# Kernel optimization log

Hardware: AMD Instinct MI355X
Metric: run time of the kernel (lower is better)

The kernel has to match this reference:

```python
import jax, jax.numpy as jnp
import numpy as np

H = 16  # number of heads (from init_kwargs)
LN_EPS = 1e-5  # torch nn.LayerNorm default


def layer_norm(x, g, b, eps=LN_EPS):
    mu = jnp.mean(x, axis=-1, keepdims=True)
    var = jnp.var(x, axis=-1, keepdims=True)
    return (x - mu) * jax.lax.rsqrt(var + eps) * g + b


def setup_inputs() -> dict:
    key = jax.random.key(0)
    ks = jax.random.split(key, 8)
    B, S, d = 2, 2048, 1024
    s = 0.02  # small init scale keeps softmax logits in a sane range
    return {
        "embed": jax.random.normal(ks[0], (B, S, d), jnp.float32),
        "Wk": jax.random.normal(ks[1], (d, d), jnp.float32) * s,
        "Wq": jax.random.normal(ks[2], (d, d), jnp.float32) * s,
        "Wv": jax.random.normal(ks[3], (d, d), jnp.float32) * s,
        "w1_w": jax.random.normal(ks[4], (4 * d, d), jnp.float32) * s,
        "w1_b": jnp.zeros((4 * d,), jnp.float32),
        "w2_w": jax.random.normal(ks[5], (d, 4 * d), jnp.float32) * s,
        "w2_b": jnp.zeros((d,), jnp.float32),
        "ln_g": jnp.ones((d,), jnp.float32),
        "ln_b": jnp.zeros((d,), jnp.float32),
        "ln2_g": jnp.ones((d,), jnp.float32),
        "ln2_b": jnp.zeros((d,), jnp.float32),
    }


def reference(embed, Wk, Wq, Wv, w1_w, w1_b, w2_w, w2_b, ln_g, ln_b, ln2_g, ln2_b):
    B, S, d = embed.shape
    dh = d // H
    # nn.Linear(d, d, bias=False): y = x @ W.T
    K = embed @ Wk.T
    Q = embed @ Wq.T
    V = embed @ Wv.T
    Qh = Q.reshape(B, S, H, dh)
    Kh = K.reshape(B, S, H, dh)
    Vh = V.reshape(B, S, H, dh)
    # per-head attention, all heads batched: [B, H, S, S]
    scores = jnp.einsum('bshd,bthd->bhst', Qh, Kh) / jnp.sqrt(jnp.float32(dh))
    attn = jax.nn.softmax(scores, axis=-1)
    out = jnp.einsum('bhst,bthd->bshd', attn, Vh).reshape(B, S, d)
    out = layer_norm(out + embed, ln_g, ln_b)          # residual + ln
    hidden = jax.nn.silu(out @ w1_w.T + w1_b)          # FFN with silu gate
    out2 = hidden @ w2_w.T + w2_b
    return layer_norm(out2 + out, ln2_g, ln2_b)        # residual + ln2
```

## Files before the change

kernel.cpp:

```cpp
#include <hip/hip_runtime.h>
#include <hip/hip_bf16.h>
#include <stdint.h>

typedef __attribute__((ext_vector_type(8))) __bf16 bf16x8;
typedef __attribute__((ext_vector_type(4))) float f32x4;
typedef __attribute__((ext_vector_type(16))) float f32x16;
typedef __attribute__((ext_vector_type(8))) uint16_t u16x8;

__device__ inline uint16_t f2bf(float x) {
  union { float f; uint32_t u; } v; v.f = x;
  uint32_t r = v.u + 0x7fffu + ((v.u >> 16) & 1u);
  return (uint16_t)(r >> 16);
}
__device__ inline float bf2f(uint16_t x) {
  union { uint32_t u; float f; } v; v.u = (uint32_t)x << 16;
  return v.f;
}

#define MFMA16(a, b, c) __builtin_amdgcn_mfma_f32_16x16x32_bf16(a, b, c, 0, 0, 0)
#define MFMA32(a, b, c) __builtin_amdgcn_mfma_f32_32x32x16_bf16(a, b, c, 0, 0, 0)
#define GLOAD16(g, l) __builtin_amdgcn_global_load_lds((const __attribute__((address_space(1))) void*)(g), (__attribute__((address_space(3))) void*)(l), 16, 0, 0)

#if __has_builtin(__builtin_amdgcn_exp2f)
#define EXP2(x) __builtin_amdgcn_exp2f(x)
#else
#define EXP2(x) exp2f(x)
#endif

__device__ inline uint32_t cvtpk_bf16(float lo, float hi) {
  uint32_t r;
  asm("v_cvt_pk_bf16_f32 %0, %1, %2" : "=v"(r) : "v"(lo), "v"(hi));
  return r;
}
__device__ inline void perm32swap(uint32_t& a, uint32_t& b) {
  asm volatile("v_permlane32_swap_b32 %0, %1" : "+v"(a), "+v"(b));
}

__global__ void cast_all(const float* __restrict__ embed, const float* __restrict__ Wq,
                         const float* __restrict__ Wk, const float* __restrict__ Wv,
                         const float* __restrict__ w1w, const float* __restrict__ w2w,
                         uint16_t* __restrict__ xbf, uint16_t* __restrict__ wqkv,
                         uint16_t* __restrict__ w1b, uint16_t* __restrict__ w2b) {
  const int i = (blockIdx.x * 256 + threadIdx.x) * 4;
  const float* src; uint16_t* dst; float sc = 1.f; int off;
  if (i < 4194304)       { src = embed; dst = xbf;            off = i; }
  else if (i < 5242880)  { src = Wq;  dst = wqkv;             off = i - 4194304; sc = 0.125f * 1.44269504f; }
  else if (i < 6291456)  { src = Wk;  dst = wqkv + 1048576;   off = i - 5242880; }
  else if (i < 7340032)  { src = Wv;  dst = wqkv + 2097152;   off = i - 6291456; }
  else if (i < 11534336) { src = w1w; dst = w1b;              off = i - 7340032; }
  else                   { src = w2w; dst = w2b;              off = i - 11534336; }
  float4 v = *(const float4*)(src + off);
  ushort4 o;
  o.x = f2bf(v.x * sc); o.y = f2bf(v.y * sc);
  o.z = f2bf(v.z * sc); o.w = f2bf(v.w * sc);
  *(ushort4*)(dst + off) = o;
}

template <int EPI>
__global__ void gemm_bt(const uint16_t* __restrict__ A, const uint16_t* __restrict__ Bm,
                        void* __restrict__ C0, void* __restrict__ C1,
                        void* __restrict__ C2, void* __restrict__ C3,
                        const float* __restrict__ bias, int N, int K, int ldk) {
  __shared__ uint16_t Albs[128 * 64];
  __shared__ uint16_t Blbs[128 * 64];
  const int tid = threadIdx.x;
  const int l = tid & 63, w = tid >> 6;
  const int wr = w >> 1, wc = w & 1;

  const int orig = blockIdx.y * gridDim.x + blockIdx.x;
  const int xcd = orig & 7;
  const int j = orig >> 3;
  const int cols_per = gridDim.y >> 1;
  const int row0 = ((xcd & 3) * 8 + (j & 7)) * 128;
  const int col0 = ((xcd >> 2) * cols_per + (j >> 3)) * 128;

  const int kz = blockIdx.z;
  const uint16_t* Ap = A + (size_t)kz * K;
  const uint16_t* Bp = Bm + (size_t)kz * K;
  void* Co = kz == 0 ? C0 : (kz == 1 ? C1 : (kz == 2 ? C2 : C3));

  const int srow8 = l >> 3;
  const int sgcol = ((l & 7) ^ srow8) * 8;
  const int lr = l & 15, l4 = l >> 4;

  f32x4 acc[4][4] = {};

  const int nk = K >> 6;
  for (int kt = 0; kt < nk; ++kt) {
    __syncthreads();
    const int k0 = kt * 64 + sgcol;
#pragma unroll
    for (int i = 0; i < 4; ++i) {
      GLOAD16(Ap + (size_t)(row0 + i * 32 + w * 8 + srow8) * ldk + k0,
              Albs + (i * 32 + w * 8) * 64);
      GLOAD16(Bp + (size_t)(col0 + i * 32 + w * 8 + srow8) * ldk + k0,
              Blbs + (i * 32 + w * 8) * 64);
    }
    __syncthreads();
#pragma unroll
    for (int kk = 0; kk < 2; ++kk) {
      bf16x8 af[4], bfr[4];
#pragma unroll
      for (int m = 0; m < 4; ++m) {
        const int r = wr * 64 + m * 16 + lr;
        af[m] = *(const bf16x8*)((const char*)Albs + r * 128 + (((kk * 4 + l4) ^ (r & 7)) << 4));
      }
#pragma unroll
      for (int n = 0; n < 4; ++n) {
        const int r = wc * 64 + n * 16 + lr;
        bfr[n] = *(const bf16x8*)((const char*)Blbs + r * 128 + (((kk * 4 + l4) ^ (r & 7)) << 4));
      }
#pragma unroll
      for (int m = 0; m < 4; ++m)
#pragma unroll
        for (int n = 0; n < 4; ++n)
          acc[m][n] = MFMA16(af[m], bfr[n], acc[m][n]);
    }
  }

  float bias_r[4];
  if (EPI == 1) {
#pragma unroll
    for (int n = 0; n < 4; ++n) bias_r[n] = bias[col0 + wc * 64 + n * 16 + lr];
  }
#pragma unroll
  for (int m = 0; m < 4; ++m)
#pragma unroll
    for (int n = 0; n < 4; ++n) {
      const int rbase = row0 + wr * 64 + m * 16 + (l4 << 2);
      const int c = col0 + wc * 64 + n * 16 + lr;
      if (EPI == 1) {
#pragma unroll
        for (int v = 0; v < 4; ++v) {
          float x = acc[m][n][v] + bias_r[n];
          float s = x / (1.f + __expf(-x));
          ((uint16_t*)Co)[(size_t)(rbase + v) * N + c] = f2bf(s);
        }
      } else if (EPI == 2) {
#pragma unroll
        for (int v = 0; v < 4; ++v)
          ((uint16_t*)Co)[(size_t)(rbase + v) * N + c] = f2bf(acc[m][n][v]);
      } else {
        if (c < 2048) {
#pragma unroll
          for (int v = 0; v < 4; ++v)
            ((uint16_t*)C0)[(size_t)(rbase + v) * 2048 + c] = f2bf(acc[m][n][v]);
        } else {
          const int d = c - 2048;
          union { uint16_t u[4]; uint64_t q; } pk;
#pragma unroll
          for (int v = 0; v < 4; ++v) pk.u[v] = f2bf(acc[m][n][v]);
          const int bb = rbase >> 11, srow = rbase & 2047;
          uint16_t* vt = (uint16_t*)C1;
          *(uint64_t*)(vt + ((size_t)((bb << 4) + (d >> 6)) * 64 + (d & 63)) * 2048 + srow) = pk.q;
        }
      }
    }
}

__global__ __launch_bounds__(256, 2) void attn_kernel(const uint16_t* __restrict__ qk,
                                                      const uint16_t* __restrict__ Vt,
                                                      uint16_t* __restrict__ Op0,
                                                      uint16_t* __restrict__ Op1,
                                                      float* __restrict__ lsum) {
  __shared__ uint16_t Klds[2][4096];
  __shared__ uint16_t Vlds[2][4096];
  const int tid = threadIdx.x;
  const int l = tid & 63, w = tid >> 6;
  const int lq = l & 31, hi = l >> 5;
  const int qt = ((blockIdx.y & 7) << 1) | (blockIdx.x >> 3);
  const int bh = ((blockIdx.x & 7) << 2) | (blockIdx.y >> 3);
  const int z = blockIdx.z;
  const size_t rowbase = (size_t)(bh >> 4) * 2048;
  const int h = bh & 15;
  const int hq = h * 64, hk = 1024 + h * 64;
  const int kvbase = z * 1024;
  uint16_t* Op = z ? Op1 : Op0;

  const int qrow = qt * 128 + w * 32 + lq;
  bf16x8 qf[4];
  {
    const uint16_t* qp = qk + (rowbase + qrow) * 2048 + hq + hi * 8;
#pragma unroll
    for (int c = 0; c < 4; ++c) qf[c] = *(const bf16x8*)(qp + c * 16);
  }

  const int srow = w * 8 + (l >> 3);
  const int gcol = 8 * ((l & 7) ^ (l >> 3));

  f32x16 ot[2];
#pragma unroll
  for (int r = 0; r < 16; ++r) { ot[0][r] = 0.f; ot[1][r] = 0.f; }
  float l_run = 0.f;

  auto STAGE = [&](int buf, int kv0) {
#pragma unroll
    for (int p = 0; p < 2; ++p) {
      const uint16_t* srcK = qk + (rowbase + kv0 + p * 32 + srow) * 2048 + hk + gcol;
      GLOAD16(srcK, (char*)&Klds[buf][0] + p * 4096 + w * 1024);
      const uint16_t* srcV = Vt + ((size_t)bh * 64 + p * 32 + srow) * 2048 + kv0 + gcol;
      GLOAD16(srcV, (char*)&Vlds[buf][0] + p * 4096 + w * 1024);
    }
  };

  STAGE(0, kvbase);
  int cur = 0;
  const int swz = (lq & 7) << 4;

  for (int t = 0; t < 16; ++t) {
    asm volatile("s_waitcnt vmcnt(0)" ::: "memory");
    __builtin_amdgcn_s_barrier();
    if (t < 15) STAGE(cur ^ 1, kvbase + (t + 1) * 64);

    f32x16 st[2];
#pragma unroll
    for (int b = 0; b < 2; ++b) {
      f32x16 acm;
#pragma unroll
      for (int r = 0; r < 16; ++r) acm[r] = 0.f;
      __builtin_amdgcn_s_setprio(1);
#pragma unroll
      for (int c = 0; c < 4; ++c) {
        const int cbk = (c * 32 + hi * 16) ^ swz;
        bf16x8 kf = *(const bf16x8*)((const char*)&Klds[cur][0] + (b * 32 + lq) * 128 + cbk);
        acm = MFMA32(kf, qf[c], acm);
      }
      __builtin_amdgcn_s_setprio(0);
      st[b] = acm;
    }

    float rsum = 0.f;
#pragma unroll
    for (int b = 0; b < 2; ++b)
#pragma unroll
      for (int r = 0; r < 16; ++r) {
        float e = EXP2(st[b][r]);
        st[b][r] = e;
        rsum += e;
      }
    l_run += rsum + __shfl_xor(rsum, 32, 64);

    uint32_t pa[4][4];
#pragma unroll
    for (int b = 0; b < 2; ++b)
#pragma unroll
      for (int c = 0; c < 2; ++c) {
        uint32_t a0 = cvtpk_bf16(st[b][8 * c + 0], st[b][8 * c + 1]);
        uint32_t a1 = cvtpk_bf16(st[b][8 * c + 2], st[b][8 * c + 3]);
        uint32_t b0 = cvtpk_bf16(st[b][8 * c + 4], st[b][8 * c + 5]);
        uint32_t b1 = cvtpk_bf16(st[b][8 * c + 6], st[b][8 * c + 7]);
        perm32swap(a0, b0);
        perm32swap(a1, b1);
        pa[b * 2 + c][0] = a0; pa[b * 2 + c][1] = a1;
        pa[b * 2 + c][2] = b0; pa[b * 2 + c][3] = b1;
      }

    __builtin_amdgcn_s_setprio(1);
#pragma unroll
    for (int ks = 0; ks < 4; ++ks) {
      bf16x8 pf = *(bf16x8*)&pa[ks][0];
#pragma unroll
      for (int db = 0; db < 2; ++db) {
        const int cbk = (ks * 32 + hi * 16) ^ swz;
        bf16x8 vf = *(const bf16x8*)((const char*)&Vlds[cur][0] + (db * 32 + lq) * 128 + cbk);
        ot[db] = MFMA32(vf, pf, ot[db]);
      }
    }
    __builtin_amdgcn_s_setprio(0);
    cur ^= 1;
  }

  uint16_t* orow = Op + (rowbase + qrow) * 1024 + h * 64;
#pragma unroll
  for (int db = 0; db < 2; ++db)
#pragma unroll
    for (int m = 0; m < 4; ++m) {
      union { uint16_t u[4]; uint64_t q; } pk;
#pragma unroll
      for (int v = 0; v < 4; ++v) pk.u[v] = f2bf(ot[db][4 * m + v]);
      *(uint64_t*)(orow + db * 32 + 8 * m + 4 * hi) = pk.q;
    }
  if (l < 32) lsum[(size_t)(z * 32 + bh) * 2048 + qrow] = l_run;
}

__global__ __launch_bounds__(256) void ln1_fused(const uint16_t* __restrict__ O0,
                                                 const uint16_t* __restrict__ O1,
                                                 const float* __restrict__ lsum,
                                                 const float* __restrict__ embed,
                                                 const float* __restrict__ g,
                                                 const float* __restrict__ b,
                                                 uint16_t* __restrict__ ybf) {
  const int row = blockIdx.x;
  const int t = threadIdx.x;
  const int l = t & 63, w = t >> 6;
  const int bb = row >> 11, q = row & 2047;
  const int bh = bb * 16 + (t >> 4);
  const float l0 = lsum[(size_t)bh * 2048 + q];
  const float l1 = lsum[(size_t)(32 + bh) * 2048 + q];
  const float linv = 1.f / (l0 + l1);
  ushort4 a = *((const ushort4*)(O0 + (size_t)row * 1024) + t);
  ushort4 c = *((const ushort4*)(O1 + (size_t)row * 1024) + t);
  float4 e = *((const float4*)(embed + (size_t)row * 1024) + t);
  float x0 = (bf2f(a.x) + bf2f(c.x)) * linv + e.x;
  float x1 = (bf2f(a.y) + bf2f(c.y)) * linv + e.y;
  float x2 = (bf2f(a.z) + bf2f(c.z)) * linv + e.z;
  float x3 = (bf2f(a.w) + bf2f(c.w)) * linv + e.w;
  float s = x0 + x1 + x2 + x3;
  float qq = x0 * x0 + x1 * x1 + x2 * x2 + x3 * x3;
#pragma unroll
  for (int off = 1; off < 64; off <<= 1) {
    s += __shfl_xor(s, off, 64);
    qq += __shfl_xor(qq, off, 64);
  }
  __shared__ float red[8];
  if (l == 0) { red[w] = s; red[w + 4] = qq; }
  __syncthreads();
  s = red[0] + red[1] + red[2] + red[3];
  qq = red[4] + red[5] + red[6] + red[7];
  const float mu = s * (1.f / 1024.f);
  const float var = qq * (1.f / 1024.f) - mu * mu;
  const float rstd = rsqrtf(var + 1e-5f);
  float4 vg = *((const float4*)g + t);
  float4 vbb = *((const float4*)b + t);
  union { uint16_t u[4]; uint64_t v; } o;
  o.u[0] = f2bf((x0 - mu) * rstd * vg.x + vbb.x);
  o.u[1] = f2bf((x1 - mu) * rstd * vg.y + vbb.y);
  o.u[2] = f2bf((x2 - mu) * rstd * vg.z + vbb.z);
  o.u[3] = f2bf((x3 - mu) * rstd * vg.w + vbb.w);
  *((uint64_t*)(ybf + (size_t)row * 1024) + t) = o.v;
}

__global__ __launch_bounds__(256) void ln_kernel(const uint16_t* __restrict__ x0b,
                                                 const uint16_t* __restrict__ xb1,
                                                 const uint16_t* __restrict__ xb2,
                                                 const uint16_t* __restrict__ xb3,
                                                 const uint16_t* __restrict__ xb4,
                                                 const float* __restrict__ abias,
                                                 const float* __restrict__ g,
                                                 const float* __restrict__ b,
                                                 float* __restrict__ y32) {
  const int row = blockIdx.x;
  const int t = threadIdx.x;
  const int l = t & 63, w = t >> 6;
  ushort4 v0 = *((const ushort4*)(x0b + (size_t)row * 1024) + t);
  float x0 = bf2f(v0.x), x1 = bf2f(v0.y), x2 = bf2f(v0.z), x3 = bf2f(v0.w);
  {
    ushort4 vb4 = *((const ushort4*)(xb1 + (size_t)row * 1024) + t);
    x0 += bf2f(vb4.x); x1 += bf2f(vb4.y); x2 += bf2f(vb4.z); x3 += bf2f(vb4.w);
  }
  {
    ushort4 vb4 = *((const ushort4*)(xb2 + (size_t)row * 1024) + t);
    x0 += bf2f(vb4.x); x1 += bf2f(vb4.y); x2 += bf2f(vb4.z); x3 += bf2f(vb4.w);
  }
  {
    ushort4 vb4 = *((const ushort4*)(xb3 + (size_t)row * 1024) + t);
    x0 += bf2f(vb4.x); x1 += bf2f(vb4.y); x2 += bf2f(vb4.z); x3 += bf2f(vb4.w);
  }
  {
    ushort4 vb4 = *((const ushort4*)(xb4 + (size_t)row * 1024) + t);
    x0 += bf2f(vb4.x); x1 += bf2f(vb4.y); x2 += bf2f(vb4.z); x3 += bf2f(vb4.w);
  }
  {
    float4 vb = *((const float4*)abias + t);
    x0 += vb.x; x1 += vb.y; x2 += vb.z; x3 += vb.w;
  }
  float s = x0 + x1 + x2 + x3;
  float q = x0 * x0 + x1 * x1 + x2 * x2 + x3 * x3;
#pragma unroll
  for (int off = 1; off < 64; off <<= 1) {
    s += __shfl_xor(s, off, 64);
    q += __shfl_xor(q, off, 64);
  }
  __shared__ float red[8];
  if (l == 0) { red[w] = s; red[w + 4] = q; }
  __syncthreads();
  s = red[0] + red[1] + red[2] + red[3];
  q = red[4] + red[5] + red[6] + red[7];
  const float mu = s * (1.f / 1024.f);
  const float var = q * (1.f / 1024.f) - mu * mu;
  const float rstd = rsqrtf(var + 1e-5f);
  float4 vg = *((const float4*)g + t);
  float4 vbb = *((const float4*)b + t);
  float y0 = (x0 - mu) * rstd * vg.x + vbb.x;
  float y1 = (x1 - mu) * rstd * vg.y + vbb.y;
  float y2 = (x2 - mu) * rstd * vg.z + vbb.z;
  float y3 = (x3 - mu) * rstd * vg.w + vbb.w;
  *((float4*)(y32 + (size_t)row * 1024) + t) = make_float4(y0, y1, y2, y3);
}

extern "C" void kernel_launch(void* const* d_in, const int* in_sizes, int n_in,
                              void* d_out, int out_size, void* d_ws, size_t ws_size,
                              hipStream_t stream) {
  const float* embed = (const float*)d_in[0];
  const float* Wk = (const float*)d_in[1];
  const float* Wq = (const float*)d_in[2];
  const float* Wv = (const float*)d_in[3];
  const float* w1w = (const float*)d_in[4];
  const float* w1bias = (const float*)d_in[5];
  const float* w2w = (const float*)d_in[6];
  const float* w2bias = (const float*)d_in[7];
  const float* lng = (const float*)d_in[8];
  const float* lnb = (const float*)d_in[9];
  const float* ln2g = (const float*)d_in[10];
  const float* ln2b = (const float*)d_in[11];

  char* ws = (char*)d_ws;
  uint16_t* qk   = (uint16_t*)(ws);
  uint16_t* abf  = (uint16_t*)(ws + 16777216);
  uint16_t* xbf  = (uint16_t*)(ws + 25165824);
  uint16_t* wqkv = (uint16_t*)(ws + 33554432);
  uint16_t* w1b  = (uint16_t*)(ws + 39845888);
  uint16_t* w2b  = (uint16_t*)(ws + 48234496);
  uint16_t* Op1  = (uint16_t*)(ws + 56623104);
  float*    lsum = (float*)(ws + 65011712);
  uint16_t* hid  = (uint16_t*)(ws + 90177536);
  uint16_t* Vt   = (uint16_t*)(ws + 90177536);
  uint16_t* part0b = (uint16_t*)(ws + 56623104);
  uint16_t* part1b = (uint16_t*)(ws);
  uint16_t* part2b = (uint16_t*)(ws + 8388608);
  uint16_t* part3b = (uint16_t*)(ws + 33554432);

  cast_all<<<dim3(15360), dim3(256), 0, stream>>>(embed, Wq, Wk, Wv, w1w, w2w,
                                                  xbf, wqkv, w1b, w2b);

  gemm_bt<3><<<dim3(32, 24), dim3(256), 0, stream>>>(xbf, wqkv, qk, Vt, nullptr, nullptr,
                                                     nullptr, 3072, 1024, 1024);
  attn_kernel<<<dim3(16, 32, 2), dim3(256), 0, stream>>>(qk, Vt, abf, Op1, lsum);
  ln1_fused<<<dim3(4096), dim3(256), 0, stream>>>(abf, Op1, lsum, embed, lng, lnb, xbf);
  gemm_bt<1><<<dim3(32, 32), dim3(256), 0, stream>>>(xbf, w1b, hid, nullptr, nullptr, nullptr,
                                                     w1bias, 4096, 1024, 1024);
  gemm_bt<2><<<dim3(32, 8, 4), dim3(256), 0, stream>>>(hid, w2b, part0b, part1b, part2b, part3b,
                                                       nullptr, 1024, 1024, 4096);
  ln_kernel<<<dim3(4096), dim3(256), 0, stream>>>(xbf, part0b, part1b, part2b, part3b,
                                                  w2bias, ln2g, ln2b, (float*)d_out);
}
```

Before: 189.7 us.

## Add 256x128-tile FFN GEMM kernel and split attention KV four ways

```diff
diff --git a/kernel.cpp b/kernel.cpp
--- a/kernel.cpp
+++ b/kernel.cpp
@@ -59,7 +59,6 @@
 template <int EPI>
 __global__ void gemm_bt(const uint16_t* __restrict__ A, const uint16_t* __restrict__ Bm,
                         void* __restrict__ C0, void* __restrict__ C1,
-                        void* __restrict__ C2, void* __restrict__ C3,
                         const float* __restrict__ bias, int N, int K, int ldk) {
   __shared__ uint16_t Albs[128 * 64];
   __shared__ uint16_t Blbs[128 * 64];
@@ -74,10 +73,8 @@
   const int row0 = ((xcd & 3) * 8 + (j & 7)) * 128;
   const int col0 = ((xcd >> 2) * cols_per + (j >> 3)) * 128;
 
-  const int kz = blockIdx.z;
-  const uint16_t* Ap = A + (size_t)kz * K;
-  const uint16_t* Bp = Bm + (size_t)kz * K;
-  void* Co = kz == 0 ? C0 : (kz == 1 ? C1 : (kz == 2 ? C2 : C3));
+  const uint16_t* Ap = A;
+  const uint16_t* Bp = Bm;
 
   const int srow8 = l >> 3;
   const int sgcol = ((l & 7) ^ srow8) * 8;
@@ -118,16 +115,105 @@
     }
   }
 
+#pragma unroll
+  for (int m = 0; m < 4; ++m)
+#pragma unroll
+    for (int n = 0; n < 4; ++n) {
+      const int rbase = row0 + wr * 64 + m * 16 + (l4 << 2);
+      const int c = col0 + wc * 64 + n * 16 + lr;
+      if (EPI == 3) {
+        if (c < 2048) {
+#pragma unroll
+          for (int v = 0; v < 4; ++v)
+            ((uint16_t*)C0)[(size_t)(rbase + v) * 2048 + c] = f2bf(acc[m][n][v]);
+        } else {
+          const int d = c - 2048;
+          union { uint16_t u[4]; uint64_t q; } pk;
+#pragma unroll
+          for (int v = 0; v < 4; ++v) pk.u[v] = f2bf(acc[m][n][v]);
+          const int bb = rbase >> 11, srow = rbase & 2047;
+          uint16_t* vt = (uint16_t*)C1;
+          *(uint64_t*)(vt + ((size_t)((bb << 4) + (d >> 6)) * 64 + (d & 63)) * 2048 + srow) = pk.q;
+        }
+      }
+    }
+}
+
+template <int EPI>
+__global__ __launch_bounds__(256, 2) void gemm_wide(
+    const uint16_t* __restrict__ A, const uint16_t* __restrict__ Bm,
+    void* __restrict__ C0, void* __restrict__ C1,
+    void* __restrict__ C2, void* __restrict__ C3,
+    const float* __restrict__ bias, int N, int K, int ldk) {
+  __shared__ uint16_t Als[256 * 64];
+  __shared__ uint16_t Bls[128 * 64];
+  const int tid = threadIdx.x;
+  const int l = tid & 63, w = tid >> 6;
+  const int wr = w >> 1, wc = w & 1;
+
+  const int orig = blockIdx.y * gridDim.x + blockIdx.x;
+  const int xcd = orig & 7;
+  const int j = orig >> 3;
+  const int rpx = gridDim.x >> 2;
+  const int cpx = gridDim.y >> 1;
+  const int row0 = ((xcd & 3) * rpx + (j % rpx)) * 256;
+  const int col0 = ((xcd >> 2) * cpx + (j / rpx)) * 128;
+
+  const int kz = blockIdx.z;
+  const uint16_t* Ap = A + (size_t)kz * K;
+  const uint16_t* Bp = Bm + (size_t)kz * K;
+  void* Co = kz == 0 ? C0 : (kz == 1 ? C1 : (kz == 2 ? C2 : C3));
+
+  const int srow8 = l >> 3;
+  const int sgcol = ((l & 7) ^ srow8) * 8;
+  const int lr = l & 15, l4 = l >> 4;
+
+  f32x4 acc[8][4] = {};
+
+  const int nk = K >> 6;
+  for (int kt = 0; kt < nk; ++kt) {
+    __syncthreads();
+    const int k0 = kt * 64 + sgcol;
+#pragma unroll
+    for (int g = 0; g < 8; ++g)
+      GLOAD16(Ap + (size_t)(row0 + g * 32 + w * 8 + srow8) * ldk + k0,
+              Als + (g * 32 + w * 8) * 64);
+#pragma unroll
+    for (int g = 0; g < 4; ++g)
+      GLOAD16(Bp + (size_t)(col0 + g * 32 + w * 8 + srow8) * ldk + k0,
+              Bls + (g * 32 + w * 8) * 64);
+    __syncthreads();
+#pragma unroll
+    for (int kk = 0; kk < 2; ++kk) {
+      bf16x8 a8[8], b4[4];
+#pragma unroll
+      for (int m = 0; m < 8; ++m) {
+        const int r = wr * 128 + m * 16 + lr;
+        a8[m] = *(const bf16x8*)((const char*)Als + r * 128 + (((kk * 4 + l4) ^ (r & 7)) << 4));
+      }
+#pragma unroll
+      for (int n = 0; n < 4; ++n) {
+        const int r = wc * 64 + n * 16 + lr;
+        b4[n] = *(const bf16x8*)((const char*)Bls + r * 128 + (((kk * 4 + l4) ^ (r & 7)) << 4));
+      }
+#pragma unroll
+      for (int m = 0; m < 8; ++m)
+#pragma unroll
+        for (int n = 0; n < 4; ++n)
+          acc[m][n] = MFMA16(a8[m], b4[n], acc[m][n]);
+    }
+  }
+
   float bias_r[4];
   if (EPI == 1) {
 #pragma unroll
     for (int n = 0; n < 4; ++n) bias_r[n] = bias[col0 + wc * 64 + n * 16 + lr];
   }
 #pragma unroll
-  for (int m = 0; m < 4; ++m)
+  for (int m = 0; m < 8; ++m)
 #pragma unroll
     for (int n = 0; n < 4; ++n) {
-      const int rbase = row0 + wr * 64 + m * 16 + (l4 << 2);
+      const int rbase = row0 + wr * 128 + m * 16 + (l4 << 2);
       const int c = col0 + wc * 64 + n * 16 + lr;
       if (EPI == 1) {
 #pragma unroll
@@ -136,24 +222,10 @@
           float s = x / (1.f + __expf(-x));
           ((uint16_t*)Co)[(size_t)(rbase + v) * N + c] = f2bf(s);
         }
-      } else if (EPI == 2) {
+      } else {
 #pragma unroll
         for (int v = 0; v < 4; ++v)
           ((uint16_t*)Co)[(size_t)(rbase + v) * N + c] = f2bf(acc[m][n][v]);
-      } else {
-        if (c < 2048) {
-#pragma unroll
-          for (int v = 0; v < 4; ++v)
-            ((uint16_t*)C0)[(size_t)(rbase + v) * 2048 + c] = f2bf(acc[m][n][v]);
-        } else {
-          const int d = c - 2048;
-          union { uint16_t u[4]; uint64_t q; } pk;
-#pragma unroll
-          for (int v = 0; v < 4; ++v) pk.u[v] = f2bf(acc[m][n][v]);
-          const int bb = rbase >> 11, srow = rbase & 2047;
-          uint16_t* vt = (uint16_t*)C1;
-          *(uint64_t*)(vt + ((size_t)((bb << 4) + (d >> 6)) * 64 + (d & 63)) * 2048 + srow) = pk.q;
-        }
       }
     }
 }
@@ -162,6 +234,8 @@
                                                       const uint16_t* __restrict__ Vt,
                                                       uint16_t* __restrict__ Op0,
                                                       uint16_t* __restrict__ Op1,
+                                                      uint16_t* __restrict__ Op2,
+                                                      uint16_t* __restrict__ Op3,
                                                       float* __restrict__ lsum) {
   __shared__ uint16_t Klds[2][4096];
   __shared__ uint16_t Vlds[2][4096];
@@ -174,8 +248,8 @@
   const size_t rowbase = (size_t)(bh >> 4) * 2048;
   const int h = bh & 15;
   const int hq = h * 64, hk = 1024 + h * 64;
-  const int kvbase = z * 1024;
-  uint16_t* Op = z ? Op1 : Op0;
+  const int kvbase = z * 512;
+  uint16_t* Op = z == 0 ? Op0 : (z == 1 ? Op1 : (z == 2 ? Op2 : Op3));
 
   const int qrow = qt * 128 + w * 32 + lq;
   bf16x8 qf[4];
@@ -207,10 +281,10 @@
   int cur = 0;
   const int swz = (lq & 7) << 4;
 
-  for (int t = 0; t < 16; ++t) {
+  for (int t = 0; t < 8; ++t) {
     asm volatile("s_waitcnt vmcnt(0)" ::: "memory");
     __builtin_amdgcn_s_barrier();
-    if (t < 15) STAGE(cur ^ 1, kvbase + (t + 1) * 64);
+    if (t < 7) STAGE(cur ^ 1, kvbase + (t + 1) * 64);
 
     f32x16 st[2];
 #pragma unroll
@@ -285,6 +359,8 @@
 
 __global__ __launch_bounds__(256) void ln1_fused(const uint16_t* __restrict__ O0,
                                                  const uint16_t* __restrict__ O1,
+                                                 const uint16_t* __restrict__ O2,
+                                                 const uint16_t* __restrict__ O3,
                                                  const float* __restrict__ lsum,
                                                  const float* __restrict__ embed,
                                                  const float* __restrict__ g,
@@ -295,16 +371,19 @@
   const int l = t & 63, w = t >> 6;
   const int bb = row >> 11, q = row & 2047;
   const int bh = bb * 16 + (t >> 4);
-  const float l0 = lsum[(size_t)bh * 2048 + q];
-  const float l1 = lsum[(size_t)(32 + bh) * 2048 + q];
-  const float linv = 1.f / (l0 + l1);
+  float lt = 0.f;
+#pragma unroll
+  for (int z = 0; z < 4; ++z) lt += lsum[(size_t)(z * 32 + bh) * 2048 + q];
+  const float linv = 1.f / lt;
   ushort4 a = *((const ushort4*)(O0 + (size_t)row * 1024) + t);
   ushort4 c = *((const ushort4*)(O1 + (size_t)row * 1024) + t);
+  ushort4 d = *((const ushort4*)(O2 + (size_t)row * 1024) + t);
+  ushort4 f = *((const ushort4*)(O3 + (size_t)row * 1024) + t);
   float4 e = *((const float4*)(embed + (size_t)row * 1024) + t);
-  float x0 = (bf2f(a.x) + bf2f(c.x)) * linv + e.x;
-  float x1 = (bf2f(a.y) + bf2f(c.y)) * linv + e.y;
-  float x2 = (bf2f(a.z) + bf2f(c.z)) * linv + e.z;
-  float x3 = (bf2f(a.w) + bf2f(c.w)) * linv + e.w;
+  float x0 = (bf2f(a.x) + bf2f(c.x) + bf2f(d.x) + bf2f(f.x)) * linv + e.x;
+  float x1 = (bf2f(a.y) + bf2f(c.y) + bf2f(d.y) + bf2f(f.y)) * linv + e.y;
+  float x2 = (bf2f(a.z) + bf2f(c.z) + bf2f(d.z) + bf2f(f.z)) * linv + e.z;
+  float x3 = (bf2f(a.w) + bf2f(c.w) + bf2f(d.w) + bf2f(f.w)) * linv + e.w;
   float s = x0 + x1 + x2 + x3;
   float qq = x0 * x0 + x1 * x1 + x2 * x2 + x3 * x3;
 #pragma unroll
@@ -406,13 +485,15 @@
 
   char* ws = (char*)d_ws;
   uint16_t* qk   = (uint16_t*)(ws);
-  uint16_t* abf  = (uint16_t*)(ws + 16777216);
+  uint16_t* Op0  = (uint16_t*)(ws + 16777216);
   uint16_t* xbf  = (uint16_t*)(ws + 25165824);
   uint16_t* wqkv = (uint16_t*)(ws + 33554432);
   uint16_t* w1b  = (uint16_t*)(ws + 39845888);
   uint16_t* w2b  = (uint16_t*)(ws + 48234496);
   uint16_t* Op1  = (uint16_t*)(ws + 56623104);
   float*    lsum = (float*)(ws + 65011712);
+  uint16_t* Op2  = (uint16_t*)(ws + 73400320);
+  uint16_t* Op3  = (uint16_t*)(ws + 81788928);
   uint16_t* hid  = (uint16_t*)(ws + 90177536);
   uint16_t* Vt   = (uint16_t*)(ws + 90177536);
   uint16_t* part0b = (uint16_t*)(ws + 56623104);
@@ -423,14 +504,15 @@
   cast_all<<<dim3(15360), dim3(256), 0, stream>>>(embed, Wq, Wk, Wv, w1w, w2w,
                                                   xbf, wqkv, w1b, w2b);
 
-  gemm_bt<3><<<dim3(32, 24), dim3(256), 0, stream>>>(xbf, wqkv, qk, Vt, nullptr, nullptr,
-                                                     nullptr, 3072, 1024, 1024);
-  attn_kernel<<<dim3(16, 32, 2), dim3(256), 0, stream>>>(qk, Vt, abf, Op1, lsum);
-  ln1_fused<<<dim3(4096), dim3(256), 0, stream>>>(abf, Op1, lsum, embed, lng, lnb, xbf);
-  gemm_bt<1><<<dim3(32, 32), dim3(256), 0, stream>>>(xbf, w1b, hid, nullptr, nullptr, nullptr,
-                                                     w1bias, 4096, 1024, 1024);
-  gemm_bt<2><<<dim3(32, 8, 4), dim3(256), 0, stream>>>(hid, w2b, part0b, part1b, part2b, part3b,
-                                                       nullptr, 1024, 1024, 4096);
+  gemm_bt<3><<<dim3(32, 24), dim3(256), 0, stream>>>(xbf, wqkv, qk, Vt, nullptr,
+                                                     3072, 1024, 1024);
+  attn_kernel<<<dim3(16, 32, 4), dim3(256), 0, stream>>>(qk, Vt, Op0, Op1, Op2, Op3, lsum);
+  ln1_fused<<<dim3(4096), dim3(256), 0, stream>>>(Op0, Op1, Op2, Op3, lsum, embed,
+                                                  lng, lnb, xbf);
+  gemm_wide<1><<<dim3(16, 32), dim3(256), 0, stream>>>(xbf, w1b, hid, nullptr, nullptr, nullptr,
+                                                       w1bias, 4096, 1024, 1024);
+  gemm_wide<2><<<dim3(16, 8, 4), dim3(256), 0, stream>>>(hid, w2b, part0b, part1b, part2b,
+                                                         part3b, nullptr, 1024, 1024, 4096);
   ln_kernel<<<dim3(4096), dim3(256), 0, stream>>>(xbf, part0b, part1b, part2b, part3b,
                                                   w2bias, ln2g, ln2b, (float*)d_out);
 }
```

Result: no change. 189.5 us (-0.1%).
